# Optimization experiments

Measured on AMD Instinct MI355X. Metric: run time of the kernel, lower is better.

## Reference

```python
import jax, jax.numpy as jnp
import numpy as np
import math

B, N, M, C, H = 4, 2048, 2048, 512, 4
D_V = C // H          # 128, used for scale and value head dim
D_QK = 2 * C // H     # 256, q/k head dim due to seq-axis split of the 2*dim qkv output
SCALE = D_V ** -0.5
EPS = 1e-12           # F.normalize eps


def _l2norm(t):
    n = jnp.linalg.norm(t, axis=-1, keepdims=True)
    return t / jnp.maximum(n, EPS)


def setup_inputs() -> dict:
    key = jax.random.key(0)
    k1, k2, k3, k4 = jax.random.split(key, 4)
    x = jax.random.normal(k1, (B, N, C), dtype=jnp.float32)
    context = jax.random.normal(k2, (B, M, C), dtype=jnp.float32)
    W_qkv = jax.random.normal(k3, (2 * C, C), dtype=jnp.float32) * 0.02  # torch Linear weight [out,in]
    W_proj = jax.random.normal(k4, (C, C), dtype=jnp.float32) * 0.02
    radius = jnp.ones((H,), dtype=jnp.float32) * math.sqrt(D_V)
    return {"x": x, "context": context, "W_qkv": W_qkv, "W_proj": W_proj, "radius": radius}


def reference(x, context, W_qkv, W_proj, radius):
    # qkv(cat([x, context], dim=1)) then split along sequence: q from x rows, k from context rows
    q = jnp.einsum('bnc,oc->bno', x, W_qkv)        # [B,N,2C]
    k = jnp.einsum('bmc,oc->bmo', context, W_qkv)  # [B,M,2C]
    q = q.reshape(B, N, H, D_QK).transpose(0, 2, 1, 3)       # [B,H,N,256]
    k = k.reshape(B, M, H, D_QK).transpose(0, 2, 1, 3)       # [B,H,M,256]
    v = context.reshape(B, M, H, D_V).transpose(0, 2, 1, 3)  # [B,H,M,128]
    r = radius[None, :, None, None]
    q = _l2norm(q) * r
    k = _l2norm(k) * r
    attn = jnp.einsum('bhnd,bhmd->bhnm', q, k) * SCALE
    attn = jax.nn.softmax(attn, axis=-1)
    out = jnp.einsum('bhnm,bhmd->bhnd', attn, v)
    out = out.transpose(0, 2, 1, 3).reshape(B, N, C)
    return jnp.einsum('bnc,oc->bno', out, W_proj)
```

## Files before the change

### kernel.cpp

```cpp
#include <hip/hip_runtime.h>
#include <hip/hip_bf16.h>
#include <stdint.h>

#define SCALE_F 0.08838834764831845f

typedef __attribute__((ext_vector_type(8))) short short8;
typedef __attribute__((ext_vector_type(4))) float f32x4;
typedef __attribute__((ext_vector_type(16))) float f32x16;
typedef __attribute__((ext_vector_type(2))) unsigned int uint2v;

__device__ __forceinline__ void g2l16(const void* g, void* l) {
  __builtin_amdgcn_global_load_lds(
      (const __attribute__((address_space(1))) void*)g,
      (__attribute__((address_space(3))) void*)l, 16, 0, 0);
}

__device__ __forceinline__ unsigned pkbf(float a, float b) {
  union { __hip_bfloat16 h[2]; unsigned u; } o;
  o.h[0] = __float2bfloat16(a); o.h[1] = __float2bfloat16(b);
  return o.u;
}

__global__ __launch_bounds__(256) void convert_all(
    const float* __restrict__ x, const float* __restrict__ ctx,
    const float* __restrict__ wqkv, const float* __restrict__ wproj,
    __hip_bfloat16* __restrict__ ab, __hip_bfloat16* __restrict__ wb,
    __hip_bfloat16* __restrict__ wpb)
{
  size_t qi = (size_t)blockIdx.x * 256 + threadIdx.x;
  const float* src; __hip_bfloat16* dst; size_t off;
  if (qi < 1048576)      { src = x;     dst = ab;           off = qi; }
  else if (qi < 2097152) { src = ctx;   dst = ab + 4194304; off = qi - 1048576; }
  else if (qi < 2228224) { src = wqkv;  dst = wb;           off = qi - 2097152; }
  else                   { src = wproj; dst = wpb;          off = qi - 2228224; }
  float4 v = ((const float4*)src)[off];
  union { __hip_bfloat16 h4[4]; uint2 u; } o;
  o.h4[0] = __float2bfloat16(v.x); o.h4[1] = __float2bfloat16(v.y);
  o.h4[2] = __float2bfloat16(v.z); o.h4[3] = __float2bfloat16(v.w);
  ((uint2*)dst)[off] = o.u;
}

__global__ __launch_bounds__(256) void transpose_v(
    const float* __restrict__ ctx, __hip_bfloat16* __restrict__ vt)
{
  __shared__ float tile[128][33];
  const int bid = blockIdx.x;
  const int mt = bid & 63;
  const int bh = bid >> 6;
  const int h = bh & 3, b = bh >> 2;
  const int tid = threadIdx.x;
  for (int i = 0; i < 16; ++i) {
    int idx = i * 256 + tid;
    int mm = idx >> 7, d = idx & 127;
    tile[d][mm] = ctx[((size_t)b * 2048 + mt * 32 + mm) * 512 + h * 128 + d];
  }
  __syncthreads();
  for (int i = 0; i < 16; ++i) {
    int idx = i * 256 + tid;
    int d = idx >> 5, mm = idx & 31;
    vt[((size_t)bh * 128 + d) * 2048 + mt * 32 + mm] = __float2bfloat16(tile[d][mm]);
  }
}

__global__ __launch_bounds__(256) void gemm_nt(
    const __hip_bfloat16* __restrict__ A, const __hip_bfloat16* __restrict__ B,
    float* __restrict__ C, int O, int K, int tiles_o)
{
  __shared__ __hip_bfloat16 sA[128 * 32];
  __shared__ __hip_bfloat16 sB[128 * 32];
  const int tid = threadIdx.x;
  const int wave = tid >> 6, lane = tid & 63;
  const int ln = lane & 15, q = lane >> 4;
  const int br = (blockIdx.x / tiles_o) * 128;
  const int bo = (blockIdx.x % tiles_o) * 128;
  const int wr = (wave >> 1) * 64, wc = (wave & 1) * 64;
  const __hip_bfloat16* Ab = A + (size_t)br * K;
  const __hip_bfloat16* Bb = B + (size_t)bo * K;
  const int row0 = tid >> 2, p0 = tid & 3;
  f32x4 acc[4][4] = {};
  for (int k0 = 0; k0 < K; k0 += 32) {
    for (int i = 0; i < 2; ++i) {
      int row = i * 64 + row0;
      g2l16(Ab + (size_t)row * K + k0 + p0 * 8, (char*)sA + (i * 256 + tid) * 16);
      g2l16(Bb + (size_t)row * K + k0 + p0 * 8, (char*)sB + (i * 256 + tid) * 16);
    }
    __syncthreads();
    short8 af[4], bfr[4];
    for (int mi = 0; mi < 4; ++mi)
      af[mi] = *(const short8*)(sA + (wr + mi * 16 + ln) * 32 + q * 8);
    for (int ni = 0; ni < 4; ++ni)
      bfr[ni] = *(const short8*)(sB + (wc + ni * 16 + ln) * 32 + q * 8);
    for (int mi = 0; mi < 4; ++mi)
      for (int ni = 0; ni < 4; ++ni)
        acc[mi][ni] = __builtin_amdgcn_mfma_f32_16x16x32_bf16(af[mi], bfr[ni], acc[mi][ni], 0, 0, 0);
    __syncthreads();
  }
  for (int mi = 0; mi < 4; ++mi)
    for (int ni = 0; ni < 4; ++ni) {
      int rg = br + wr + mi * 16 + q * 4;
      int cg = bo + wc + ni * 16 + ln;
      for (int r = 0; r < 4; ++r)
        C[(size_t)(rg + r) * O + cg] = acc[mi][ni][r];
    }
}

__global__ __launch_bounds__(256) void normalize_qk(
    const float* __restrict__ proj, const float* __restrict__ radius,
    __hip_bfloat16* __restrict__ qn, __hip_bfloat16* __restrict__ kn)
{
  const int r = blockIdx.x;
  const int h = threadIdx.x >> 6, lane = threadIdx.x & 63;
  float4 v = *(const float4*)(proj + (size_t)r * 1024 + h * 256 + lane * 4);
  float ss = v.x * v.x + v.y * v.y + v.z * v.z + v.w * v.w;
  for (int off = 1; off < 64; off <<= 1) ss += __shfl_xor(ss, off);
  float nrm = fmaxf(sqrtf(ss), 1e-12f);
  const bool isq = r < 8192;
  const int rr = isq ? r : r - 8192;
  const float rad = radius[h];
  const float sc = (isq ? rad * rad * SCALE_F : 1.0f) / nrm;
  __hip_bfloat16* dst = (isq ? qn : kn) +
      ((size_t)((rr >> 11) * 4 + h) * 2048 + (rr & 2047)) * 256 + lane * 4;
  union { __hip_bfloat16 h4[4]; uint2 u; } o;
  o.h4[0] = __float2bfloat16(v.x * sc);
  o.h4[1] = __float2bfloat16(v.y * sc);
  o.h4[2] = __float2bfloat16(v.z * sc);
  o.h4[3] = __float2bfloat16(v.w * sc);
  *(uint2*)dst = o.u;
}

__global__ __launch_bounds__(256, 2) void attn(
    const __hip_bfloat16* __restrict__ qn,
    const __hip_bfloat16* __restrict__ kn,
    const __hip_bfloat16* __restrict__ vt,
    float* __restrict__ Op,
    float* __restrict__ den)
{
  __shared__ __hip_bfloat16 sK[2][32 * 256];
  __shared__ __hip_bfloat16 sV[2][128 * 32];
  const int tid = threadIdx.x, wave = tid >> 6, lane = tid & 63;
  const int m32 = lane & 31, hi = lane >> 5;
  const int i = blockIdx.x;
  const int bh = (i & 7) + 8 * ((i >> 3) & 1);
  const int half = (i >> 4) & 1;
  const int nt = i >> 5;
  const int mbase = half * 1024;
  const __hip_bfloat16* Q = qn + ((size_t)bh * 2048 + nt * 128 + wave * 32) * 256;
  const __hip_bfloat16* Kp = kn + (size_t)bh * 2048 * 256;
  const __hip_bfloat16* Vp = vt + (size_t)bh * 128 * 2048;

  short8 qf[16];
  for (int kk = 0; kk < 16; ++kk)
    qf[kk] = *(const short8*)(Q + m32 * 256 + kk * 16 + hi * 8);

  f32x16 oacc[4];
  for (int v = 0; v < 4; ++v)
    for (int j = 0; j < 16; ++j) oacc[v][j] = 0.f;
  float denom = 0.f;

  for (int t = 0; t < 4; ++t) {
    int D = t * 256 + tid, row = D >> 5, cc = D & 31;
    g2l16(Kp + (size_t)(mbase + row) * 256 + ((cc ^ (row & 7)) << 3),
          (char*)sK[0] + D * 16);
  }
  for (int t = 0; t < 2; ++t) {
    int D = t * 256 + tid, rd = D >> 2, cc = D & 3;
    g2l16(Vp + (size_t)rd * 2048 + mbase + ((cc ^ ((rd >> 1) & 3)) << 3),
          (char*)sV[0] + D * 16);
  }
  __syncthreads();

  for (int it = 0; it < 32; ++it) {
    const int cur = it & 1, nxt = cur ^ 1;
    if (it + 1 < 32) {
      const int m1 = mbase + (it + 1) * 32;
      for (int t = 0; t < 4; ++t) {
        int D = t * 256 + tid, row = D >> 5, cc = D & 31;
        g2l16(Kp + (size_t)(m1 + row) * 256 + ((cc ^ (row & 7)) << 3),
              (char*)sK[nxt] + D * 16);
      }
      for (int t = 0; t < 2; ++t) {
        int D = t * 256 + tid, rd = D >> 2, cc = D & 3;
        g2l16(Vp + (size_t)rd * 2048 + m1 + ((cc ^ ((rd >> 1) & 3)) << 3),
              (char*)sV[nxt] + D * 16);
      }
    }
    const __hip_bfloat16* sKc = sK[cur];
    f32x16 sa, sb;
    for (int j = 0; j < 16; ++j) { sa[j] = 0.f; sb[j] = 0.f; }
#pragma unroll
    for (int kk = 0; kk < 8; ++kk) {
      int ca = kk * 2 + hi, cb = (kk + 8) * 2 + hi;
      short8 kfa = *(const short8*)(sKc + m32 * 256 + ((ca ^ (m32 & 7)) << 3));
      short8 kfb = *(const short8*)(sKc + m32 * 256 + ((cb ^ (m32 & 7)) << 3));
      sa = __builtin_amdgcn_mfma_f32_32x32x16_bf16(kfa, qf[kk], sa, 0, 0, 0);
      sb = __builtin_amdgcn_mfma_f32_32x32x16_bf16(kfb, qf[kk + 8], sb, 0, 0, 0);
    }
    float p_[16];
#pragma unroll
    for (int reg = 0; reg < 16; ++reg) {
      float e = __expf(sa[reg] + sb[reg]);
      denom += e;
      p_[reg] = e;
    }
    uint2v s0 = __builtin_amdgcn_permlane32_swap(pkbf(p_[0], p_[1]),  pkbf(p_[4],  p_[5]),  false, false);
    uint2v s1 = __builtin_amdgcn_permlane32_swap(pkbf(p_[2], p_[3]),  pkbf(p_[6],  p_[7]),  false, false);
    uint2v s2 = __builtin_amdgcn_permlane32_swap(pkbf(p_[8], p_[9]),  pkbf(p_[12], p_[13]), false, false);
    uint2v s3 = __builtin_amdgcn_permlane32_swap(pkbf(p_[10], p_[11]), pkbf(p_[14], p_[15]), false, false);
    union { unsigned u[4]; short8 s; } ua, ub;
    ua.u[0] = s0.x; ua.u[1] = s1.x; ua.u[2] = s0.y; ua.u[3] = s1.y;
    ub.u[0] = s2.x; ub.u[1] = s3.x; ub.u[2] = s2.y; ub.u[3] = s3.y;
    const __hip_bfloat16* sVc = sV[cur];
#pragma unroll
    for (int kc = 0; kc < 2; ++kc) {
      short8 pf = kc ? ub.s : ua.s;
#pragma unroll
      for (int vi = 0; vi < 4; ++vi) {
        int rd = vi * 32 + m32;
        int c = kc * 2 + hi;
        short8 vf = *(const short8*)(sVc + rd * 32 + ((c ^ ((rd >> 1) & 3)) << 3));
        oacc[vi] = __builtin_amdgcn_mfma_f32_32x32x16_bf16(vf, pf, oacc[vi], 0, 0, 0);
      }
    }
    __syncthreads();
  }

  float dfull = denom + __shfl_xor(denom, 32);
  float* Opb = Op + (size_t)(half * 16 + bh) * 2048 * 128;
  float* denb = den + (size_t)(half * 16 + bh) * 2048;
  const int rbase = nt * 128 + wave * 32;
  if (hi == 0) denb[rbase + m32] = dfull;
  float* sc_ = (float*)(&sK[0][0]) + wave * 1056;
#pragma unroll
  for (int vi = 0; vi < 4; ++vi) {
#pragma unroll
    for (int reg = 0; reg < 16; ++reg) {
      int dL = (reg & 3) + 8 * (reg >> 2) + 4 * hi;
      sc_[m32 * 33 + dL] = oacc[vi][reg];
    }
    asm volatile("s_waitcnt lgkmcnt(0)" ::: "memory");
#pragma unroll
    for (int qq = 0; qq < 16; ++qq) {
      int qr = qq * 2 + hi;
      Opb[(size_t)(rbase + qr) * 128 + vi * 32 + m32] = sc_[qr * 33 + m32];
    }
    asm volatile("s_waitcnt lgkmcnt(0)" ::: "memory");
  }
}

__global__ __launch_bounds__(256) void combine(
    const float* __restrict__ Op, const float* __restrict__ den,
    __hip_bfloat16* __restrict__ ob)
{
  int qi = blockIdx.x * 256 + threadIdx.x;
  int r = qi >> 5;
  int dq = qi & 31;
  int bh = r >> 11, n = r & 2047, b = bh >> 2, h = bh & 3;
  float4 o0 = ((const float4*)Op)[qi];
  float4 o1 = ((const float4*)(Op + 4194304))[qi];
  float inv = 1.0f / (den[r] + den[32768 + r]);
  union { __hip_bfloat16 h4[4]; uint2 u; } o;
  o.h4[0] = __float2bfloat16((o0.x + o1.x) * inv);
  o.h4[1] = __float2bfloat16((o0.y + o1.y) * inv);
  o.h4[2] = __float2bfloat16((o0.z + o1.z) * inv);
  o.h4[3] = __float2bfloat16((o0.w + o1.w) * inv);
  *(uint2*)&ob[((size_t)b * 2048 + n) * 512 + h * 128 + dq * 4] = o.u;
}

extern "C" void kernel_launch(void* const* d_in, const int* in_sizes, int n_in,
                              void* d_out, int out_size, void* d_ws, size_t ws_size,
                              hipStream_t stream) {
  const float* x      = (const float*)d_in[0];
  const float* ctx    = (const float*)d_in[1];
  const float* wqkv   = (const float*)d_in[2];
  const float* wproj  = (const float*)d_in[3];
  const float* radius = (const float*)d_in[4];
  char* ws = (char*)d_ws;
  __hip_bfloat16* ab  = (__hip_bfloat16*)(ws);
  __hip_bfloat16* wb  = (__hip_bfloat16*)(ws + 16777216);
  __hip_bfloat16* wpb = (__hip_bfloat16*)(ws + 17825792);
  float*          proj= (float*)(ws + 18350080);
  float*          Op  = proj;
  float*          den = (float*)(ws + 18350080 + 33554432);
  __hip_bfloat16* qn  = (__hip_bfloat16*)(ws + 85458944);
  __hip_bfloat16* kn  = (__hip_bfloat16*)(ws + 102236160);
  __hip_bfloat16* vt  = (__hip_bfloat16*)(ws + 119013376);
  __hip_bfloat16* ob  = (__hip_bfloat16*)(ws + 127401984);
  float* out = (float*)d_out;

  convert_all<<<8960, 256, 0, stream>>>(x, ctx, wqkv, wproj, ab, wb, wpb);
  transpose_v<<<1024, 256, 0, stream>>>(ctx, vt);
  gemm_nt<<<1024, 256, 0, stream>>>(ab, wb, proj, 1024, 512, 8);
  normalize_qk<<<16384, 256, 0, stream>>>(proj, radius, qn, kn);
  attn<<<512, 256, 0, stream>>>(qn, kn, vt, Op, den);
  combine<<<4096, 256, 0, stream>>>(Op, den, ob);
  gemm_nt<<<256, 256, 0, stream>>>(ob, wpb, out, 512, 512, 4);
}
```

Before: 223.1 us.

## Split attention keys four ways and read V directly from global memory

The attention kernel now splits the key dimension into four quarters instead of two, doubling the grid to 1024 blocks. It drops the LDS staging of V and loads V fragments straight from global memory, and it raises launch bounds to 3 blocks per CU. The exp/pack code is interleaved to cut register pressure. The combine kernel now sums four partials, and the denominator buffer moves to the start of the workspace. This trades more partial-output traffic and uncached global V reads for more parallelism and occupancy.

```diff
diff --git a/kernel.cpp b/kernel.cpp
--- a/kernel.cpp
+++ b/kernel.cpp
@@ -128,7 +128,7 @@
   *(uint2*)dst = o.u;
 }
 
-__global__ __launch_bounds__(256, 2) void attn(
+__global__ __launch_bounds__(256, 3) void attn(
     const __hip_bfloat16* __restrict__ qn,
     const __hip_bfloat16* __restrict__ kn,
     const __hip_bfloat16* __restrict__ vt,
@@ -136,14 +136,14 @@
     float* __restrict__ den)
 {
   __shared__ __hip_bfloat16 sK[2][32 * 256];
-  __shared__ __hip_bfloat16 sV[2][128 * 32];
   const int tid = threadIdx.x, wave = tid >> 6, lane = tid & 63;
   const int m32 = lane & 31, hi = lane >> 5;
   const int i = blockIdx.x;
   const int bh = (i & 7) + 8 * ((i >> 3) & 1);
-  const int half = (i >> 4) & 1;
-  const int nt = i >> 5;
-  const int mbase = half * 1024;
+  const int r4 = i >> 4;
+  const int qtr = r4 & 3;
+  const int nt = r4 >> 2;
+  const int mbase = qtr * 512;
   const __hip_bfloat16* Q = qn + ((size_t)bh * 2048 + nt * 128 + wave * 32) * 256;
   const __hip_bfloat16* Kp = kn + (size_t)bh * 2048 * 256;
   const __hip_bfloat16* Vp = vt + (size_t)bh * 128 * 2048;
@@ -162,27 +162,17 @@
     g2l16(Kp + (size_t)(mbase + row) * 256 + ((cc ^ (row & 7)) << 3),
           (char*)sK[0] + D * 16);
   }
-  for (int t = 0; t < 2; ++t) {
-    int D = t * 256 + tid, rd = D >> 2, cc = D & 3;
-    g2l16(Vp + (size_t)rd * 2048 + mbase + ((cc ^ ((rd >> 1) & 3)) << 3),
-          (char*)sV[0] + D * 16);
-  }
   __syncthreads();
 
-  for (int it = 0; it < 32; ++it) {
+  for (int it = 0; it < 16; ++it) {
     const int cur = it & 1, nxt = cur ^ 1;
-    if (it + 1 < 32) {
+    if (it + 1 < 16) {
       const int m1 = mbase + (it + 1) * 32;
       for (int t = 0; t < 4; ++t) {
         int D = t * 256 + tid, row = D >> 5, cc = D & 31;
         g2l16(Kp + (size_t)(m1 + row) * 256 + ((cc ^ (row & 7)) << 3),
               (char*)sK[nxt] + D * 16);
       }
-      for (int t = 0; t < 2; ++t) {
-        int D = t * 256 + tid, rd = D >> 2, cc = D & 3;
-        g2l16(Vp + (size_t)rd * 2048 + m1 + ((cc ^ ((rd >> 1) & 3)) << 3),
-              (char*)sV[nxt] + D * 16);
-      }
     }
     const __hip_bfloat16* sKc = sK[cur];
     f32x16 sa, sb;
@@ -195,29 +185,41 @@
       sa = __builtin_amdgcn_mfma_f32_32x32x16_bf16(kfa, qf[kk], sa, 0, 0, 0);
       sb = __builtin_amdgcn_mfma_f32_32x32x16_bf16(kfb, qf[kk + 8], sb, 0, 0, 0);
     }
-    float p_[16];
-#pragma unroll
-    for (int reg = 0; reg < 16; ++reg) {
-      float e = __expf(sa[reg] + sb[reg]);
-      denom += e;
-      p_[reg] = e;
-    }
-    uint2v s0 = __builtin_amdgcn_permlane32_swap(pkbf(p_[0], p_[1]),  pkbf(p_[4],  p_[5]),  false, false);
-    uint2v s1 = __builtin_amdgcn_permlane32_swap(pkbf(p_[2], p_[3]),  pkbf(p_[6],  p_[7]),  false, false);
-    uint2v s2 = __builtin_amdgcn_permlane32_swap(pkbf(p_[8], p_[9]),  pkbf(p_[12], p_[13]), false, false);
-    uint2v s3 = __builtin_amdgcn_permlane32_swap(pkbf(p_[10], p_[11]), pkbf(p_[14], p_[15]), false, false);
     union { unsigned u[4]; short8 s; } ua, ub;
-    ua.u[0] = s0.x; ua.u[1] = s1.x; ua.u[2] = s0.y; ua.u[3] = s1.y;
-    ub.u[0] = s2.x; ub.u[1] = s3.x; ub.u[2] = s2.y; ub.u[3] = s3.y;
-    const __hip_bfloat16* sVc = sV[cur];
+    {
+      float e0, e1, e2, e3;
+      unsigned u0, u1, u2, u3;
+      e0 = __expf(sa[0] + sb[0]); e1 = __expf(sa[1] + sb[1]);
+      e2 = __expf(sa[2] + sb[2]); e3 = __expf(sa[3] + sb[3]);
+      denom += (e0 + e1) + (e2 + e3);
+      u0 = pkbf(e0, e1); u1 = pkbf(e2, e3);
+      e0 = __expf(sa[4] + sb[4]); e1 = __expf(sa[5] + sb[5]);
+      e2 = __expf(sa[6] + sb[6]); e3 = __expf(sa[7] + sb[7]);
+      denom += (e0 + e1) + (e2 + e3);
+      u2 = pkbf(e0, e1); u3 = pkbf(e2, e3);
+      uint2v s0 = __builtin_amdgcn_permlane32_swap(u0, u2, false, false);
+      uint2v s1 = __builtin_amdgcn_permlane32_swap(u1, u3, false, false);
+      ua.u[0] = s0.x; ua.u[1] = s1.x; ua.u[2] = s0.y; ua.u[3] = s1.y;
+      e0 = __expf(sa[8] + sb[8]);   e1 = __expf(sa[9] + sb[9]);
+      e2 = __expf(sa[10] + sb[10]); e3 = __expf(sa[11] + sb[11]);
+      denom += (e0 + e1) + (e2 + e3);
+      u0 = pkbf(e0, e1); u1 = pkbf(e2, e3);
+      e0 = __expf(sa[12] + sb[12]); e1 = __expf(sa[13] + sb[13]);
+      e2 = __expf(sa[14] + sb[14]); e3 = __expf(sa[15] + sb[15]);
+      denom += (e0 + e1) + (e2 + e3);
+      u2 = pkbf(e0, e1); u3 = pkbf(e2, e3);
+      uint2v s2 = __builtin_amdgcn_permlane32_swap(u0, u2, false, false);
+      uint2v s3 = __builtin_amdgcn_permlane32_swap(u1, u3, false, false);
+      ub.u[0] = s2.x; ub.u[1] = s3.x; ub.u[2] = s2.y; ub.u[3] = s3.y;
+    }
+    const __hip_bfloat16* Vb = Vp + mbase + it * 32;
 #pragma unroll
     for (int kc = 0; kc < 2; ++kc) {
       short8 pf = kc ? ub.s : ua.s;
 #pragma unroll
       for (int vi = 0; vi < 4; ++vi) {
-        int rd = vi * 32 + m32;
-        int c = kc * 2 + hi;
-        short8 vf = *(const short8*)(sVc + rd * 32 + ((c ^ ((rd >> 1) & 3)) << 3));
+        short8 vf = *(const short8*)(Vb + (size_t)(vi * 32 + m32) * 2048 +
+                                     (kc * 2 + hi) * 8);
         oacc[vi] = __builtin_amdgcn_mfma_f32_32x32x16_bf16(vf, pf, oacc[vi], 0, 0, 0);
       }
     }
@@ -225,8 +227,8 @@
   }
 
   float dfull = denom + __shfl_xor(denom, 32);
-  float* Opb = Op + (size_t)(half * 16 + bh) * 2048 * 128;
-  float* denb = den + (size_t)(half * 16 + bh) * 2048;
+  float* Opb = Op + (size_t)(qtr * 16 + bh) * 2048 * 128;
+  float* denb = den + (size_t)(qtr * 16 + bh) * 2048;
   const int rbase = nt * 128 + wave * 32;
   if (hi == 0) denb[rbase + m32] = dfull;
   float* sc_ = (float*)(&sK[0][0]) + wave * 1056;
@@ -257,12 +259,14 @@
   int bh = r >> 11, n = r & 2047, b = bh >> 2, h = bh & 3;
   float4 o0 = ((const float4*)Op)[qi];
   float4 o1 = ((const float4*)(Op + 4194304))[qi];
-  float inv = 1.0f / (den[r] + den[32768 + r]);
+  float4 o2 = ((const float4*)(Op + 8388608))[qi];
+  float4 o3 = ((const float4*)(Op + 12582912))[qi];
+  float inv = 1.0f / (den[r] + den[32768 + r] + den[65536 + r] + den[98304 + r]);
   union { __hip_bfloat16 h4[4]; uint2 u; } o;
-  o.h4[0] = __float2bfloat16((o0.x + o1.x) * inv);
-  o.h4[1] = __float2bfloat16((o0.y + o1.y) * inv);
-  o.h4[2] = __float2bfloat16((o0.z + o1.z) * inv);
-  o.h4[3] = __float2bfloat16((o0.w + o1.w) * inv);
+  o.h4[0] = __float2bfloat16((o0.x + o1.x + o2.x + o3.x) * inv);
+  o.h4[1] = __float2bfloat16((o0.y + o1.y + o2.y + o3.y) * inv);
+  o.h4[2] = __float2bfloat16((o0.z + o1.z + o2.z + o3.z) * inv);
+  o.h4[3] = __float2bfloat16((o0.w + o1.w + o2.w + o3.w) * inv);
   *(uint2*)&ob[((size_t)b * 2048 + n) * 512 + h * 128 + dq * 4] = o.u;
 }
 
@@ -280,7 +284,7 @@
   __hip_bfloat16* wpb = (__hip_bfloat16*)(ws + 17825792);
   float*          proj= (float*)(ws + 18350080);
   float*          Op  = proj;
-  float*          den = (float*)(ws + 18350080 + 33554432);
+  float*          den = (float*)(ws);
   __hip_bfloat16* qn  = (__hip_bfloat16*)(ws + 85458944);
   __hip_bfloat16* kn  = (__hip_bfloat16*)(ws + 102236160);
   __hip_bfloat16* vt  = (__hip_bfloat16*)(ws + 119013376);
@@ -291,7 +295,7 @@
   transpose_v<<<1024, 256, 0, stream>>>(ctx, vt);
   gemm_nt<<<1024, 256, 0, stream>>>(ab, wb, proj, 1024, 512, 8);
   normalize_qk<<<16384, 256, 0, stream>>>(proj, radius, qn, kn);
-  attn<<<512, 256, 0, stream>>>(qn, kn, vt, Op, den);
+  attn<<<1024, 256, 0, stream>>>(qn, kn, vt, Op, den);
   combine<<<4096, 256, 0, stream>>>(Op, den, ob);
   gemm_nt<<<256, 256, 0, stream>>>(ob, wpb, out, 512, 512, 4);
 }
```

New measurement: 379.2 us. +70.0%, slower.

## Prefetch two KV tiles ahead with vmcnt waits and MFMA priority hints

Applied to the files above, without the earlier changes.

Restructures the attention main loop so the K/V tile for iteration it+2 is issued right after the barrier that ends iteration it. Each iteration now waits with s_waitcnt vmcnt(6) for the current tile instead of using a full __syncthreads drain. It also raises wave priority around the MFMA blocks and interleaves exp, pack and permlane steps to shorten register live ranges. The aim is to hide global-to-LDS latency better and cut barrier stalls. The cost is reliance on exact vmcnt accounting with the direct-to-LDS loads, which is fragile if the compiler reorders or adds memory ops.

```diff
diff --git a/kernel.cpp b/kernel.cpp
--- a/kernel.cpp
+++ b/kernel.cpp
@@ -128,6 +128,24 @@
   *(uint2*)dst = o.u;
 }
 
+__device__ __forceinline__ void stage_kv(
+    const __hip_bfloat16* __restrict__ Kp, const __hip_bfloat16* __restrict__ Vp,
+    int mrow, __hip_bfloat16* dK, __hip_bfloat16* dV, int tid)
+{
+#pragma unroll
+  for (int t = 0; t < 4; ++t) {
+    int D = t * 256 + tid, row = D >> 5, cc = D & 31;
+    g2l16(Kp + (size_t)(mrow + row) * 256 + ((cc ^ (row & 7)) << 3),
+          (char*)dK + D * 16);
+  }
+#pragma unroll
+  for (int t = 0; t < 2; ++t) {
+    int D = t * 256 + tid, rd = D >> 2, cc = D & 3;
+    g2l16(Vp + (size_t)rd * 2048 + mrow + ((cc ^ ((rd >> 1) & 3)) << 3),
+          (char*)dV + D * 16);
+  }
+}
+
 __global__ __launch_bounds__(256, 2) void attn(
     const __hip_bfloat16* __restrict__ qn,
     const __hip_bfloat16* __restrict__ kn,
@@ -149,44 +167,29 @@
   const __hip_bfloat16* Vp = vt + (size_t)bh * 128 * 2048;
 
   short8 qf[16];
+#pragma unroll
   for (int kk = 0; kk < 16; ++kk)
     qf[kk] = *(const short8*)(Q + m32 * 256 + kk * 16 + hi * 8);
+  asm volatile("s_waitcnt vmcnt(0)" ::: "memory");
 
   f32x16 oacc[4];
   for (int v = 0; v < 4; ++v)
     for (int j = 0; j < 16; ++j) oacc[v][j] = 0.f;
   float denom = 0.f;
 
-  for (int t = 0; t < 4; ++t) {
-    int D = t * 256 + tid, row = D >> 5, cc = D & 31;
-    g2l16(Kp + (size_t)(mbase + row) * 256 + ((cc ^ (row & 7)) << 3),
-          (char*)sK[0] + D * 16);
-  }
-  for (int t = 0; t < 2; ++t) {
-    int D = t * 256 + tid, rd = D >> 2, cc = D & 3;
-    g2l16(Vp + (size_t)rd * 2048 + mbase + ((cc ^ ((rd >> 1) & 3)) << 3),
-          (char*)sV[0] + D * 16);
-  }
-  __syncthreads();
+  stage_kv(Kp, Vp, mbase,      sK[0], sV[0], tid);
+  stage_kv(Kp, Vp, mbase + 32, sK[1], sV[1], tid);
 
   for (int it = 0; it < 32; ++it) {
-    const int cur = it & 1, nxt = cur ^ 1;
-    if (it + 1 < 32) {
-      const int m1 = mbase + (it + 1) * 32;
-      for (int t = 0; t < 4; ++t) {
-        int D = t * 256 + tid, row = D >> 5, cc = D & 31;
-        g2l16(Kp + (size_t)(m1 + row) * 256 + ((cc ^ (row & 7)) << 3),
-              (char*)sK[nxt] + D * 16);
-      }
-      for (int t = 0; t < 2; ++t) {
-        int D = t * 256 + tid, rd = D >> 2, cc = D & 3;
-        g2l16(Vp + (size_t)rd * 2048 + m1 + ((cc ^ ((rd >> 1) & 3)) << 3),
-              (char*)sV[nxt] + D * 16);
-      }
-    }
+    const int cur = it & 1;
+    if (it < 31) asm volatile("s_waitcnt vmcnt(6)" ::: "memory");
+    else         asm volatile("s_waitcnt vmcnt(0)" ::: "memory");
+    __builtin_amdgcn_s_barrier();
+
     const __hip_bfloat16* sKc = sK[cur];
     f32x16 sa, sb;
     for (int j = 0; j < 16; ++j) { sa[j] = 0.f; sb[j] = 0.f; }
+    __builtin_amdgcn_s_setprio(1);
 #pragma unroll
     for (int kk = 0; kk < 8; ++kk) {
       int ca = kk * 2 + hi, cb = (kk + 8) * 2 + hi;
@@ -195,21 +198,36 @@
       sa = __builtin_amdgcn_mfma_f32_32x32x16_bf16(kfa, qf[kk], sa, 0, 0, 0);
       sb = __builtin_amdgcn_mfma_f32_32x32x16_bf16(kfb, qf[kk + 8], sb, 0, 0, 0);
     }
-    float p_[16];
-#pragma unroll
-    for (int reg = 0; reg < 16; ++reg) {
-      float e = __expf(sa[reg] + sb[reg]);
-      denom += e;
-      p_[reg] = e;
-    }
-    uint2v s0 = __builtin_amdgcn_permlane32_swap(pkbf(p_[0], p_[1]),  pkbf(p_[4],  p_[5]),  false, false);
-    uint2v s1 = __builtin_amdgcn_permlane32_swap(pkbf(p_[2], p_[3]),  pkbf(p_[6],  p_[7]),  false, false);
-    uint2v s2 = __builtin_amdgcn_permlane32_swap(pkbf(p_[8], p_[9]),  pkbf(p_[12], p_[13]), false, false);
-    uint2v s3 = __builtin_amdgcn_permlane32_swap(pkbf(p_[10], p_[11]), pkbf(p_[14], p_[15]), false, false);
+    __builtin_amdgcn_s_setprio(0);
     union { unsigned u[4]; short8 s; } ua, ub;
-    ua.u[0] = s0.x; ua.u[1] = s1.x; ua.u[2] = s0.y; ua.u[3] = s1.y;
-    ub.u[0] = s2.x; ub.u[1] = s3.x; ub.u[2] = s2.y; ub.u[3] = s3.y;
+    {
+      float e0, e1, e2, e3;
+      unsigned u0, u1, u2, u3;
+      e0 = __expf(sa[0] + sb[0]); e1 = __expf(sa[1] + sb[1]);
+      e2 = __expf(sa[2] + sb[2]); e3 = __expf(sa[3] + sb[3]);
+      denom += (e0 + e1) + (e2 + e3);
+      u0 = pkbf(e0, e1); u1 = pkbf(e2, e3);
+      e0 = __expf(sa[4] + sb[4]); e1 = __expf(sa[5] + sb[5]);
+      e2 = __expf(sa[6] + sb[6]); e3 = __expf(sa[7] + sb[7]);
+      denom += (e0 + e1) + (e2 + e3);
+      u2 = pkbf(e0, e1); u3 = pkbf(e2, e3);
+      uint2v s0 = __builtin_amdgcn_permlane32_swap(u0, u2, false, false);
+      uint2v s1 = __builtin_amdgcn_permlane32_swap(u1, u3, false, false);
+      ua.u[0] = s0.x; ua.u[1] = s1.x; ua.u[2] = s0.y; ua.u[3] = s1.y;
+      e0 = __expf(sa[8] + sb[8]);   e1 = __expf(sa[9] + sb[9]);
+      e2 = __expf(sa[10] + sb[10]); e3 = __expf(sa[11] + sb[11]);
+      denom += (e0 + e1) + (e2 + e3);
+      u0 = pkbf(e0, e1); u1 = pkbf(e2, e3);
+      e0 = __expf(sa[12] + sb[12]); e1 = __expf(sa[13] + sb[13]);
+      e2 = __expf(sa[14] + sb[14]); e3 = __expf(sa[15] + sb[15]);
+      denom += (e0 + e1) + (e2 + e3);
+      u2 = pkbf(e0, e1); u3 = pkbf(e2, e3);
+      uint2v s2 = __builtin_amdgcn_permlane32_swap(u0, u2, false, false);
+      uint2v s3 = __builtin_amdgcn_permlane32_swap(u1, u3, false, false);
+      ub.u[0] = s2.x; ub.u[1] = s3.x; ub.u[2] = s2.y; ub.u[3] = s3.y;
+    }
     const __hip_bfloat16* sVc = sV[cur];
+    __builtin_amdgcn_s_setprio(1);
 #pragma unroll
     for (int kc = 0; kc < 2; ++kc) {
       short8 pf = kc ? ub.s : ua.s;
@@ -221,7 +239,11 @@
         oacc[vi] = __builtin_amdgcn_mfma_f32_32x32x16_bf16(vf, pf, oacc[vi], 0, 0, 0);
       }
     }
-    __syncthreads();
+    __builtin_amdgcn_s_setprio(0);
+
+    __builtin_amdgcn_s_barrier();
+    if (it + 2 < 32)
+      stage_kv(Kp, Vp, mbase + (it + 2) * 32, sK[cur], sV[cur], tid);
   }
 
   float dfull = denom + __shfl_xor(denom, 32);
```

After: 227.6 us. Within noise of the previous version (+2.0%).
